# Kernel optimization log

Hardware: AMD Instinct MI355X
Metric: run time of the kernel (lower is better)

## Reference

```python
import jax, jax.numpy as jnp
import numpy as np
from jax import lax

SEQ, BATCH, IN, HID, LAYERS = 512, 64, 512, 1024, 2


def _uniform(key, shape, scale):
    return jax.random.uniform(key, shape, jnp.float32, -scale, scale)


def setup_inputs() -> dict:
    key = jax.random.key(0)
    ks = jax.random.split(key, 16)
    scale = 1.0 / np.sqrt(HID)
    inp = {
        "x": jax.random.normal(ks[0], (SEQ, BATCH, IN), jnp.float32),
        "h0": jnp.zeros((LAYERS, BATCH, HID), jnp.float32),
        "c0": jnp.zeros((LAYERS, BATCH, HID), jnp.float32),
    }
    in_sizes = [IN, HID]
    for l in range(LAYERS):
        base = 1 + 4 * l
        inp[f"w_ih_{l}"] = _uniform(ks[base + 0], (4 * HID, in_sizes[l]), scale)
        inp[f"w_hh_{l}"] = _uniform(ks[base + 1], (4 * HID, HID), scale)
        inp[f"b_ih_{l}"] = _uniform(ks[base + 2], (4 * HID,), scale)
        inp[f"b_hh_{l}"] = _uniform(ks[base + 3], (4 * HID,), scale)
    return inp


def _lstm_layer(x_seq, h0, c0, w_ih, w_hh, b_ih, b_hh):
    # x_seq: [S, B, D_in]; returns ys: [S, B, H], final (h, c)
    def step(carry, x_t):
        h, c = carry
        gates = x_t @ w_ih.T + b_ih + h @ w_hh.T + b_hh  # [B, 4H]
        i, f, g, o = jnp.split(gates, 4, axis=-1)
        i = jax.nn.sigmoid(i)
        f = jax.nn.sigmoid(f)
        g = jnp.tanh(g)
        o = jax.nn.sigmoid(o)
        c_new = f * c + i * g
        h_new = o * jnp.tanh(c_new)
        return (h_new, c_new), h_new

    (hT, cT), ys = lax.scan(step, (h0, c0), x_seq)
    return ys, hT, cT


def reference(x, h0, c0, w_ih_0, w_hh_0, b_ih_0, b_hh_0,
              w_ih_1, w_hh_1, b_ih_1, b_hh_1):
    # Layer 0
    y0, h_f0, c_f0 = _lstm_layer(x, h0[0], c0[0], w_ih_0, w_hh_0, b_ih_0, b_hh_0)
    # Layer 1 consumes layer-0 hidden sequence
    y1, h_f1, c_f1 = _lstm_layer(y0, h0[1], c0[1], w_ih_1, w_hh_1, b_ih_1, b_hh_1)
    hn = jnp.stack([h_f0, h_f1], axis=0)  # [layers, B, H]
    cn = jnp.stack([c_f0, c_f1], axis=0)
    return y1, hn, cn
```

## Files before the change

kernel.cpp:

```cpp
#include <hip/hip_runtime.h>
#include <hip/hip_bf16.h>
#include <cstdint>


typedef __attribute__((ext_vector_type(8))) short short8;
typedef __attribute__((ext_vector_type(4))) short short4b;
typedef __attribute__((ext_vector_type(4))) float f32x4;

#define AS1 __attribute__((address_space(1)))
#define AS3 __attribute__((address_space(3)))

static __device__ __forceinline__ void gload_lds16(const void* g, void* l) {
  __builtin_amdgcn_global_load_lds((const AS1 unsigned int*)g, (AS3 unsigned int*)l,
                                   16, 0, 0);
}

static __device__ __forceinline__ float sigmoidf_(float x) {
  return 1.f / (1.f + __expf(-x));
}

static __device__ __forceinline__ float bf2f(short s) {
  union { unsigned u; float f; } v;
  v.u = ((unsigned)(unsigned short)s) << 16;
  return v.f;
}

static __device__ __forceinline__ unsigned f2bfbits(float f) {
  __hip_bfloat16 h = __float2bfloat16(f);
  union { __hip_bfloat16 h; unsigned short u; } v;
  v.h = h;
  return (unsigned)v.u;
}

static __device__ __forceinline__ f32x4 ld16_llc(const void* p) {
  f32x4 r;
  asm volatile("global_load_dwordx4 %0, %1, off sc0 sc1" : "=v"(r) : "v"(p) : "memory");
  return r;
}
static __device__ __forceinline__ uint2 ld8_llc(const void* p) {
  uint2 r;
  asm volatile("global_load_dwordx2 %0, %1, off sc0 sc1" : "=v"(r) : "v"(p) : "memory");
  return r;
}
static __device__ __forceinline__ void st16_llc(void* p, f32x4 v) {
  asm volatile("global_store_dwordx4 %0, %1, off sc0 sc1" :: "v"(p), "v"(v) : "memory");
}
static __device__ __forceinline__ void st4_llc(void* p, unsigned v) {
  asm volatile("global_store_dword %0, %1, off sc0 sc1" :: "v"(p), "v"(v) : "memory");
}

static __device__ __forceinline__ void stage32(const char* src, char* smem, int tid) {
  f32x4 tmp[8];
#pragma unroll
  for (int i = 0; i < 8; ++i)
    tmp[i] = ld16_llc(src + (size_t)(i * 512 + tid) * 16);
  asm volatile("s_waitcnt vmcnt(0)" ::: "memory");
#pragma unroll
  for (int i = 0; i < 8; ++i) {
    int bo = (i * 512 + tid) * 16;
    int row = bo >> 11;
    *(f32x4*)(smem + (bo ^ ((row & 7) << 4))) = tmp[i];
  }
}

static __device__ __forceinline__ void arrive_flag(unsigned* slot, unsigned val, int tid) {
  asm volatile("s_waitcnt vmcnt(0)" ::: "memory");
  __syncthreads();
  if (tid == 0) st4_llc(slot, val);
}

static __device__ __forceinline__ void pollf(const unsigned* f, unsigned tgt, int lane) {
  const unsigned* a = f + (lane & 31) * 32;
  while (__hip_atomic_load(a, __ATOMIC_RELAXED, __HIP_MEMORY_SCOPE_AGENT) < tgt) {
  }
}

__global__ void cvt_bf16(const float* __restrict__ in, __hip_bfloat16* __restrict__ out,
                         int n4) {
  int i = blockIdx.x * 256 + threadIdx.x;
  if (i >= n4) return;
  float4 v = ((const float4*)in)[i];
  out[i * 4 + 0] = __float2bfloat16(v.x);
  out[i * 4 + 1] = __float2bfloat16(v.y);
  out[i * 4 + 2] = __float2bfloat16(v.z);
  out[i * 4 + 3] = __float2bfloat16(v.w);
}

__global__ void cvt_permrow(const float* __restrict__ in, __hip_bfloat16* __restrict__ out,
                            int K) {
  int k4 = blockIdx.x * 256 + threadIdx.x;
  if (k4 >= (K >> 2)) return;
  int rp = blockIdx.y;
  int src = (rp & 3) * 1024 + (rp >> 2);
  float4 v = ((const float4*)(in + (size_t)src * K))[k4];
  __hip_bfloat16* o = out + (size_t)rp * K + k4 * 4;
  o[0] = __float2bfloat16(v.x);
  o[1] = __float2bfloat16(v.y);
  o[2] = __float2bfloat16(v.z);
  o[3] = __float2bfloat16(v.w);
}

__global__ void bias_perm(const float* __restrict__ b1, const float* __restrict__ b2,
                          float* __restrict__ o) {
  int i = blockIdx.x * 256 + threadIdx.x;
  if (i >= 4096) return;
  int src = (i & 3) * 1024 + (i >> 2);
  o[i] = b1[src] + b2[src];
}

__global__ void init_state(const float* __restrict__ h0, const float* __restrict__ c0,
                           __hip_bfloat16* __restrict__ h_init, float* __restrict__ c_state,
                           int n) {
  int i = blockIdx.x * 256 + threadIdx.x;
  if (i >= n) return;
  h_init[i] = __float2bfloat16(h0[i]);
  c_state[i] = c0[i];
}

__global__ void finalize_out(const float* __restrict__ hf, const float* __restrict__ cst,
                             float* __restrict__ out_h, float* __restrict__ out_c, int n) {
  int i = blockIdx.x * 256 + threadIdx.x;
  if (i >= n) return;
  out_h[i] = hf[i];
  out_c[i] = cst[i];
}

__global__ __launch_bounds__(256) void gemm_bt_bias(
    const __hip_bfloat16* __restrict__ A, const __hip_bfloat16* __restrict__ B,
    __hip_bfloat16* __restrict__ C, const float* __restrict__ bias, int K, int N) {
  const int tid = threadIdx.x;
  const int lane = tid & 63;
  const int wv = tid >> 6;
  const int l15 = lane & 15, l4 = lane >> 4;
  const int bm = blockIdx.x * 128;
  const int bn = blockIdx.y * 128;
  __shared__ alignas(16) __hip_bfloat16 As[128 * 64];
  __shared__ alignas(16) __hip_bfloat16 Bs[128 * 64];
  f32x4 acc[4][4] = {};
  const int wm = (wv >> 1) * 64;
  const int wn = (wv & 1) * 64;

  for (int kt = 0; kt < K; kt += 64) {
    if (kt) __syncthreads();
#pragma unroll
    for (int it = 0; it < 4; ++it) {
      int ci = it * 256 + tid;
      int row = ci >> 3, c8 = ci & 7;
      gload_lds16(A + (bm + row) * K + kt + c8 * 8, As + (it * 256 + wv * 64) * 8);
      gload_lds16(B + (bn + row) * K + kt + c8 * 8, Bs + (it * 256 + wv * 64) * 8);
    }
    __syncthreads();
#pragma unroll
    for (int kk = 0; kk < 64; kk += 32) {
      short8 a[4], b[4];
#pragma unroll
      for (int m = 0; m < 4; ++m)
        a[m] = *(const short8*)(As + (wm + m * 16 + l15) * 64 + kk + l4 * 8);
#pragma unroll
      for (int n = 0; n < 4; ++n)
        b[n] = *(const short8*)(Bs + (wn + n * 16 + l15) * 64 + kk + l4 * 8);
#pragma unroll
      for (int m = 0; m < 4; ++m)
#pragma unroll
        for (int n = 0; n < 4; ++n)
          acc[m][n] = __builtin_amdgcn_mfma_f32_16x16x32_bf16(a[m], b[n], acc[m][n], 0, 0, 0);
    }
  }
#pragma unroll
  for (int n = 0; n < 4; ++n) {
    int col = bn + wn + n * 16 + l15;
    float bs = bias[col];
#pragma unroll
    for (int m = 0; m < 4; ++m) {
#pragma unroll
      for (int j = 0; j < 4; ++j) {
        int row = bm + wm + m * 16 + l4 * 4 + j;
        C[(size_t)row * N + col] = __float2bfloat16(acc[m][n][j] + bs);
      }
    }
  }
}

__global__ __launch_bounds__(512, 1) void lstm_pipeline(
    const __hip_bfloat16* __restrict__ Gin,
    const __hip_bfloat16* __restrict__ Whh0,
    const __hip_bfloat16* __restrict__ Whh1,
    const __hip_bfloat16* __restrict__ Wih1,
    const float* __restrict__ bias1,
    const __hip_bfloat16* __restrict__ hinit,
    __hip_bfloat16* __restrict__ y0b,
    __hip_bfloat16* __restrict__ gring,
    __hip_bfloat16* __restrict__ h1r,
    float* __restrict__ yout,
    float* __restrict__ cst,
    float* __restrict__ hf,
    unsigned* __restrict__ ctrs) {
  extern __shared__ char smem[];
  const int tid = threadIdx.x;
  const int lane = tid & 63;
  const int wv = tid >> 6;
  const int l15 = lane & 15, l4 = lane >> 4;
  const int bid = blockIdx.x;
  const int pipe = bid >= 96;
  const int wid = pipe ? bid - 96 : bid;
  const int gbat = pipe * 32;
  __hip_bfloat16* xp = (__hip_bfloat16*)(smem + 65536);
  unsigned* l0f = ctrs + pipe * 3072;
  unsigned* pf  = l0f + 1024;
  unsigned* l1f = l0f + 2048;
  __hip_bfloat16* y0p = y0b + (size_t)pipe * 512 * 32768;
  __hip_bfloat16* grp_ = gring + (size_t)pipe * 1048576;
  __hip_bfloat16* h1p = h1r + (size_t)pipe * 65536;

  if (wid < 32) {
    const int m = wid;
    const int bbase = m * 32;
    const int hid = bbase + wv * 4 + l4;
    const int grow = (l15 & 3) * 1024 + bbase + wv * 4 + (l15 >> 2);
    const __hip_bfloat16* wrow = Whh0 + (size_t)grow * 1024 + l4 * 8;
    short8 a[32];
#pragma unroll
    for (int kk = 0; kk < 32; ++kk) a[kk] = *(const short8*)(wrow + kk * 32);
#pragma unroll
    for (int kk = 0; kk < 32; ++kk) asm volatile("" : "+v"(a[kk]));

    float cS[2];
#pragma unroll
    for (int s = 0; s < 2; ++s)
      cS[s] = cst[(gbat + s * 16 + l15) * 1024 + hid];

    short4b gv0 = *(const short4b*)(Gin + (gbat + l15) * 4096 + hid * 4);
    short4b gv1 = *(const short4b*)(Gin + (gbat + 16 + l15) * 4096 + hid * 4);

    for (int t = 0; t < 512; ++t) {
      stage32(t ? (const char*)(y0p + (size_t)(t - 1) * 32768)
                : (const char*)(hinit + (size_t)gbat * 1024),
              smem, tid);
      __syncthreads();

      f32x4 acc[2][4] = {};
#pragma unroll
      for (int kk = 0; kk < 32; ++kk) {
        int ko = kk * 64 + l4 * 16;
#pragma unroll
        for (int s = 0; s < 2; ++s) {
          int bl = s * 16 + l15;
          short8 b = *(const short8*)(smem + ((bl * 2048 + ko) ^ ((bl & 7) << 4)));
          acc[s][kk & 3] =
              __builtin_amdgcn_mfma_f32_16x16x32_bf16(a[kk], b, acc[s][kk & 3], 0, 0, 0);
        }
      }

#pragma unroll
      for (int s = 0; s < 2; ++s) {
        int bl = s * 16 + l15;
        int bat = gbat + bl;
        const short4b gv = s ? gv1 : gv0;
        float gi = acc[s][0][0] + acc[s][1][0] + acc[s][2][0] + acc[s][3][0] + bf2f(gv[0]);
        float gf = acc[s][0][1] + acc[s][1][1] + acc[s][2][1] + acc[s][3][1] + bf2f(gv[1]);
        float gg = acc[s][0][2] + acc[s][1][2] + acc[s][2][2] + acc[s][3][2] + bf2f(gv[2]);
        float go = acc[s][0][3] + acc[s][1][3] + acc[s][2][3] + acc[s][3][3] + bf2f(gv[3]);
        float i_ = sigmoidf_(gi);
        float f_ = sigmoidf_(gf);
        float g_ = tanhf(gg);
        float o_ = sigmoidf_(go);
        cS[s] = f_ * cS[s] + i_ * g_;
        float h = o_ * tanhf(cS[s]);
        xp[bl * 32 + wv * 4 + l4] = __float2bfloat16(h);
        if (t == 511) {
          hf[bat * 1024 + hid] = h;
          cst[bat * 1024 + hid] = cS[s];
        }
      }
      __syncthreads();
      if (tid < 128) {
        int b_ = tid >> 2, part = tid & 3;
        f32x4 v = *(const f32x4*)(xp + b_ * 32 + part * 8);
        st16_llc(y0p + (size_t)t * 32768 + b_ * 1024 + bbase + part * 8, v);
      }
      arrive_flag(l0f + m * 32, (unsigned)(t + 1), tid);
      if (t < 511) {
        gv0 = *(const short4b*)(Gin + (size_t)(t + 1) * 262144 + (gbat + l15) * 4096 + hid * 4);
        gv1 = *(const short4b*)(Gin + (size_t)(t + 1) * 262144 + (gbat + 16 + l15) * 4096 + hid * 4);
        if (tid < 64) pollf(l0f, (unsigned)(t + 1), lane);
        __syncthreads();
      }
    }

  } else if (wid < 64) {
    const int pp = wid - 32;
    const int bbase = pp * 32;
    const int hid = bbase + wv * 4 + l4;
    const int grow = (l15 & 3) * 1024 + bbase + wv * 4 + (l15 >> 2);
    const __hip_bfloat16* wrow = Wih1 + (size_t)grow * 1024 + l4 * 8;
    short8 a[32];
#pragma unroll
    for (int kk = 0; kk < 32; ++kk) a[kk] = *(const short8*)(wrow + kk * 32);
#pragma unroll
    for (int kk = 0; kk < 32; ++kk) asm volatile("" : "+v"(a[kk]));

    const f32x4 bv = *(const f32x4*)(bias1 + hid * 4);

    for (int t = 0; t < 512; ++t) {
      if (tid < 64) pollf(l0f, (unsigned)(t + 1), lane);
      else if (tid < 128 && t >= 6) pollf(l1f, (unsigned)(t - 5), lane);
      __syncthreads();

      stage32((const char*)(y0p + (size_t)t * 32768), smem, tid);
      __syncthreads();

      f32x4 acc[2][4] = {};
#pragma unroll
      for (int kk = 0; kk < 32; ++kk) {
        int ko = kk * 64 + l4 * 16;
#pragma unroll
        for (int s = 0; s < 2; ++s) {
          int bl = s * 16 + l15;
          short8 b = *(const short8*)(smem + ((bl * 2048 + ko) ^ ((bl & 7) << 4)));
          acc[s][kk & 3] =
              __builtin_amdgcn_mfma_f32_16x16x32_bf16(a[kk], b, acc[s][kk & 3], 0, 0, 0);
        }
      }

#pragma unroll
      for (int s = 0; s < 2; ++s) {
        int bl = s * 16 + l15;
        float g0 = acc[s][0][0] + acc[s][1][0] + acc[s][2][0] + acc[s][3][0] + bv[0];
        float g1 = acc[s][0][1] + acc[s][1][1] + acc[s][2][1] + acc[s][3][1] + bv[1];
        float g2 = acc[s][0][2] + acc[s][1][2] + acc[s][2][2] + acc[s][3][2] + bv[2];
        float g3 = acc[s][0][3] + acc[s][1][3] + acc[s][2][3] + acc[s][3][3] + bv[3];
        uint2 u;
        u.x = f2bfbits(g0) | (f2bfbits(g1) << 16);
        u.y = f2bfbits(g2) | (f2bfbits(g3) << 16);
        *(uint2*)(xp + bl * 128 + (wv * 4 + l4) * 4) = u;
      }
      __syncthreads();
      {
        __hip_bfloat16* gdst = grp_ + (size_t)(t & 7) * 131072;
        int b_ = tid >> 4, part = tid & 15;
        f32x4 v = *(const f32x4*)(xp + b_ * 128 + part * 8);
        st16_llc(gdst + (size_t)b_ * 4096 + bbase * 4 + part * 8, v);
      }
      arrive_flag(pf + pp * 32, (unsigned)(t + 1), tid);
    }

  } else {
    const int j = wid - 64;
    const int bbase = j * 32;
    const int hid = bbase + wv * 4 + l4;
    const int grow = (l15 & 3) * 1024 + bbase + wv * 4 + (l15 >> 2);
    const __hip_bfloat16* wrow = Whh1 + (size_t)grow * 1024 + l4 * 8;
    short8 a[32];
#pragma unroll
    for (int kk = 0; kk < 32; ++kk) a[kk] = *(const short8*)(wrow + kk * 32);
#pragma unroll
    for (int kk = 0; kk < 32; ++kk) asm volatile("" : "+v"(a[kk]));

    float cS[2];
#pragma unroll
    for (int s = 0; s < 2; ++s)
      cS[s] = cst[65536 + (gbat + s * 16 + l15) * 1024 + hid];

    for (int t = 0; t < 512; ++t) {
      if (tid < 64) pollf(pf, (unsigned)(t + 1), lane);
      else if (tid < 128 && t >= 1) pollf(l1f, (unsigned)t, lane);
      __syncthreads();

      const __hip_bfloat16* gsrc = grp_ + (size_t)(t & 7) * 131072;
      uint2 gu[2];
#pragma unroll
      for (int s = 0; s < 2; ++s)
        gu[s] = ld8_llc(gsrc + (size_t)(s * 16 + l15) * 4096 + hid * 4);
      stage32(t ? (const char*)(h1p + (size_t)((t - 1) & 1) * 32768)
                : (const char*)(hinit + 65536 + (size_t)gbat * 1024),
              smem, tid);
      __syncthreads();

      f32x4 acc[2][4] = {};
#pragma unroll
      for (int kk = 0; kk < 32; ++kk) {
        int ko = kk * 64 + l4 * 16;
#pragma unroll
        for (int s = 0; s < 2; ++s) {
          int bl = s * 16 + l15;
          short8 b = *(const short8*)(smem + ((bl * 2048 + ko) ^ ((bl & 7) << 4)));
          acc[s][kk & 3] =
              __builtin_amdgcn_mfma_f32_16x16x32_bf16(a[kk], b, acc[s][kk & 3], 0, 0, 0);
        }
      }

#pragma unroll
      for (int s = 0; s < 2; ++s) {
        int bl = s * 16 + l15;
        int bat = gbat + bl;
        union { uint2 u; short ss[4]; } gp;
        gp.u = gu[s];
        float gi = acc[s][0][0] + acc[s][1][0] + acc[s][2][0] + acc[s][3][0] + bf2f(gp.ss[0]);
        float gf = acc[s][0][1] + acc[s][1][1] + acc[s][2][1] + acc[s][3][1] + bf2f(gp.ss[1]);
        float gg = acc[s][0][2] + acc[s][1][2] + acc[s][2][2] + acc[s][3][2] + bf2f(gp.ss[2]);
        float go = acc[s][0][3] + acc[s][1][3] + acc[s][2][3] + acc[s][3][3] + bf2f(gp.ss[3]);
        float i_ = sigmoidf_(gi);
        float f_ = sigmoidf_(gf);
        float g_ = tanhf(gg);
        float o_ = sigmoidf_(go);
        cS[s] = f_ * cS[s] + i_ * g_;
        float h = o_ * tanhf(cS[s]);
        xp[bl * 32 + wv * 4 + l4] = __float2bfloat16(h);
        if (t == 511) {
          hf[65536 + bat * 1024 + hid] = h;
          cst[65536 + bat * 1024 + hid] = cS[s];
        }
      }
      __syncthreads();
      if (tid < 128) {
        int b_ = tid >> 2, part = tid & 3;
        f32x4 v = *(const f32x4*)(xp + b_ * 32 + part * 8);
        st16_llc(h1p + (size_t)(t & 1) * 32768 + b_ * 1024 + bbase + part * 8, v);
      }
      arrive_flag(l1f + j * 32, (unsigned)(t + 1), tid);

      if (tid < 256) {
        int b_ = tid >> 3, part = tid & 7;
        short4b hv = *(const short4b*)(xp + b_ * 32 + part * 4);
        f32x4 v;
        v[0] = bf2f(hv[0]); v[1] = bf2f(hv[1]); v[2] = bf2f(hv[2]); v[3] = bf2f(hv[3]);
        *(f32x4*)(yout + (size_t)t * 65536 + (size_t)(gbat + b_) * 1024 + bbase + part * 4) = v;
      }
    }
  }
}

extern "C" void kernel_launch(void* const* d_in, const int* in_sizes, int n_in,
                              void* d_out_, int out_size, void* d_ws, size_t ws_size,
                              hipStream_t stream) {
  (void)in_sizes; (void)n_in; (void)out_size; (void)ws_size;
  const float* x      = (const float*)d_in[0];
  const float* h0     = (const float*)d_in[1];
  const float* c0     = (const float*)d_in[2];
  const float* w_ih_0 = (const float*)d_in[3];
  const float* w_hh_0 = (const float*)d_in[4];
  const float* b_ih_0 = (const float*)d_in[5];
  const float* b_hh_0 = (const float*)d_in[6];
  const float* w_ih_1 = (const float*)d_in[7];
  const float* w_hh_1 = (const float*)d_in[8];
  const float* b_ih_1 = (const float*)d_in[9];
  const float* b_hh_1 = (const float*)d_in[10];
  float* out = (float*)d_out_;

  char* p = (char*)d_ws;
  auto alloc = [&](size_t bytes) { char* r = p; p += (bytes + 255) & ~(size_t)255; return r; };
  __hip_bfloat16* xb    = (__hip_bfloat16*)alloc(33554432);
  __hip_bfloat16* wbih0 = (__hip_bfloat16*)alloc(4194304);
  __hip_bfloat16* wbhh0 = (__hip_bfloat16*)alloc(8388608);
  __hip_bfloat16* wbih1 = (__hip_bfloat16*)alloc(8388608);
  __hip_bfloat16* wbhh1 = (__hip_bfloat16*)alloc(8388608);
  __hip_bfloat16* y0b   = (__hip_bfloat16*)alloc(67108864);
  __hip_bfloat16* Gin   = (__hip_bfloat16*)alloc(268435456);
  __hip_bfloat16* gring = (__hip_bfloat16*)alloc(4194304);
  __hip_bfloat16* h1r   = (__hip_bfloat16*)alloc(262144);
  __hip_bfloat16* hinit = (__hip_bfloat16*)alloc(262144);
  float* bsum0          = (float*)alloc(16384);
  float* bsum1          = (float*)alloc(16384);
  float* cst            = (float*)alloc(524288);
  float* hf             = (float*)alloc(524288);
  unsigned* ctrs        = (unsigned*)alloc(32768);

  (void)hipFuncSetAttribute((const void*)lstm_pipeline,
                            hipFuncAttributeMaxDynamicSharedMemorySize, 73728);

  cvt_bf16<<<16777216 / 4 / 256, 256, 0, stream>>>(x, xb, 16777216 / 4);
  cvt_permrow<<<dim3(1, 4096), 256, 0, stream>>>(w_ih_0, wbih0, 512);
  cvt_bf16<<<4194304 / 4 / 256, 256, 0, stream>>>(w_hh_0, wbhh0, 4194304 / 4);
  cvt_bf16<<<4194304 / 4 / 256, 256, 0, stream>>>(w_ih_1, wbih1, 4194304 / 4);
  cvt_bf16<<<4194304 / 4 / 256, 256, 0, stream>>>(w_hh_1, wbhh1, 4194304 / 4);
  bias_perm<<<16, 256, 0, stream>>>(b_ih_0, b_hh_0, bsum0);
  bias_perm<<<16, 256, 0, stream>>>(b_ih_1, b_hh_1, bsum1);
  init_state<<<131072 / 256, 256, 0, stream>>>(h0, c0, hinit, cst, 131072);
  (void)hipMemsetAsync(ctrs, 0, 32768, stream);

  gemm_bt_bias<<<dim3(256, 32), 256, 0, stream>>>(xb, wbih0, Gin, bsum0, 512, 4096);

  {
    const __hip_bfloat16* g_ = Gin;
    const __hip_bfloat16* w0_ = wbhh0;
    const __hip_bfloat16* w1_ = wbhh1;
    const __hip_bfloat16* wi_ = wbih1;
    const float* b1_ = bsum1;
    const __hip_bfloat16* hi_ = hinit;
    __hip_bfloat16* y0_ = y0b;
    __hip_bfloat16* gr_ = gring;
    __hip_bfloat16* h1_ = h1r;
    float* yo_ = out;
    float* c_ = cst;
    float* hf_ = hf;
    unsigned* ct_ = ctrs;
    void* args[] = {&g_, &w0_, &w1_, &wi_, &b1_, &hi_, &y0_, &gr_, &h1_,
                    &yo_, &c_, &hf_, &ct_};
    (void)hipLaunchCooperativeKernel((void*)lstm_pipeline, dim3(192), dim3(512),
                                     args, 73728, stream);
  }

  finalize_out<<<131072 / 256, 256, 0, stream>>>(hf, cst, out + 33554432, out + 33685504, 131072);
}
```

Before: 3.828 ms.

## Replace block-wide flag polling with per-wave polling of needed producer slices

Each wave now stages only the hidden-state slice written by four specific producer blocks, and polls only those four flags before loading it. This removes the global poll-then-__syncthreads barrier that waited for all 32 producers before any staging could begin. The projection-consumer waits only on its own producer flag. Each wave can start loading as soon as its slices are ready, at the cost of a more complex staging layout and less obvious memory ordering between flags and data.

Result: slower. 4.733 ms (+23.6%).

```diff
diff --git a/kernel.cpp b/kernel.cpp
--- a/kernel.cpp
+++ b/kernel.cpp
@@ -49,17 +49,35 @@
   asm volatile("global_store_dword %0, %1, off sc0 sc1" :: "v"(p), "v"(v) : "memory");
 }
 
-static __device__ __forceinline__ void stage32(const char* src, char* smem, int tid) {
+static __device__ __forceinline__ void stage32w(const char* src, const unsigned* f,
+                                                unsigned tgt, char* smem, int tid) {
+  const int wv = tid >> 6;
+  const int lane = tid & 63;
+  if (f) {
+    const unsigned* a = f + (wv * 4 + (lane & 3)) * 32;
+    for (;;) {
+      unsigned v = (lane < 4)
+          ? __hip_atomic_load(a, __ATOMIC_RELAXED, __HIP_MEMORY_SCOPE_AGENT)
+          : tgt;
+      if (!__ballot(v < tgt)) break;
+    }
+  }
   f32x4 tmp[8];
 #pragma unroll
-  for (int i = 0; i < 8; ++i)
-    tmp[i] = ld16_llc(src + (size_t)(i * 512 + tid) * 16);
+  for (int it = 0; it < 8; ++it) {
+    int c = it * 64 + lane;
+    int row = c >> 4;
+    int part = (c & 15) ^ (row & 7);
+    tmp[it] = ld16_llc(src + row * 2048 + wv * 256 + part * 16);
+  }
   asm volatile("s_waitcnt vmcnt(0)" ::: "memory");
 #pragma unroll
-  for (int i = 0; i < 8; ++i) {
-    int bo = (i * 512 + tid) * 16;
-    int row = bo >> 11;
-    *(f32x4*)(smem + (bo ^ ((row & 7) << 4))) = tmp[i];
+  for (int it = 0; it < 8; ++it) {
+    int c = it * 64 + lane;
+    int row = c >> 4;
+    int part = (c & 15) ^ (row & 7);
+    int bo = row * 2048 + wv * 256 + part * 16;
+    *(f32x4*)(smem + (bo ^ ((row & 7) << 4))) = tmp[it];
   }
 }
 
@@ -233,9 +251,9 @@
     short4b gv1 = *(const short4b*)(Gin + (gbat + 16 + l15) * 4096 + hid * 4);
 
     for (int t = 0; t < 512; ++t) {
-      stage32(t ? (const char*)(y0p + (size_t)(t - 1) * 32768)
-                : (const char*)(hinit + (size_t)gbat * 1024),
-              smem, tid);
+      stage32w(t ? (const char*)(y0p + (size_t)(t - 1) * 32768)
+                 : (const char*)(hinit + (size_t)gbat * 1024),
+               t ? l0f : nullptr, (unsigned)t, smem, tid);
       __syncthreads();
 
       f32x4 acc[2][4] = {};
@@ -282,8 +300,6 @@
       if (t < 511) {
         gv0 = *(const short4b*)(Gin + (size_t)(t + 1) * 262144 + (gbat + l15) * 4096 + hid * 4);
         gv1 = *(const short4b*)(Gin + (size_t)(t + 1) * 262144 + (gbat + 16 + l15) * 4096 + hid * 4);
-        if (tid < 64) pollf(l0f, (unsigned)(t + 1), lane);
-        __syncthreads();
       }
     }
 
@@ -302,11 +318,9 @@
     const f32x4 bv = *(const f32x4*)(bias1 + hid * 4);
 
     for (int t = 0; t < 512; ++t) {
-      if (tid < 64) pollf(l0f, (unsigned)(t + 1), lane);
-      else if (tid < 128 && t >= 6) pollf(l1f, (unsigned)(t - 5), lane);
-      __syncthreads();
-
-      stage32((const char*)(y0p + (size_t)t * 32768), smem, tid);
+      if (t >= 6 && tid >= 64 && tid < 128) pollf(l1f, (unsigned)(t - 5), lane);
+      stage32w((const char*)(y0p + (size_t)t * 32768), l0f, (unsigned)(t + 1),
+               smem, tid);
       __syncthreads();
 
       f32x4 acc[2][4] = {};
@@ -362,18 +376,17 @@
       cS[s] = cst[65536 + (gbat + s * 16 + l15) * 1024 + hid];
 
     for (int t = 0; t < 512; ++t) {
-      if (tid < 64) pollf(pf, (unsigned)(t + 1), lane);
-      else if (tid < 128 && t >= 1) pollf(l1f, (unsigned)t, lane);
-      __syncthreads();
-
+      while (__hip_atomic_load(pf + j * 32, __ATOMIC_RELAXED,
+                               __HIP_MEMORY_SCOPE_AGENT) < (unsigned)(t + 1)) {
+      }
       const __hip_bfloat16* gsrc = grp_ + (size_t)(t & 7) * 131072;
       uint2 gu[2];
 #pragma unroll
       for (int s = 0; s < 2; ++s)
         gu[s] = ld8_llc(gsrc + (size_t)(s * 16 + l15) * 4096 + hid * 4);
-      stage32(t ? (const char*)(h1p + (size_t)((t - 1) & 1) * 32768)
-                : (const char*)(hinit + 65536 + (size_t)gbat * 1024),
-              smem, tid);
+      stage32w(t ? (const char*)(h1p + (size_t)((t - 1) & 1) * 32768)
+                 : (const char*)(hinit + 65536 + (size_t)gbat * 1024),
+               t ? l1f : nullptr, (unsigned)t, smem, tid);
       __syncthreads();
 
       f32x4 acc[2][4] = {};
```
